# Kernel tuning notes

Hardware: AMD Instinct MI355X
Metric: run time of the kernel (lower is better)

## Reference

```python
import math
import jax, jax.numpy as jnp
import numpy as np

NUM_HEADS = 16
NUM_BUCKETS = 32
MAX_DISTANCE = 128
NEG_INF = -1e9
LN_EPS = 1e-5


def _rel_pos_bias(rab_emb, T):
    # buckets for relative position (i - j) clamped at 0, T5-style log buckets
    i = jnp.arange(T)[:, None]
    j = jnp.arange(T)[None, :]
    n = jnp.clip(i - j, 0, None)  # = -(mem - ctx), clamped min 0
    max_exact = NUM_BUCKETS // 2
    large = max_exact + (
        jnp.log(n.astype(jnp.float32) / max_exact + 1e-6)
        / math.log(MAX_DISTANCE / max_exact)
        * (NUM_BUCKETS - max_exact)
    ).astype(jnp.int32)
    large = jnp.minimum(large, NUM_BUCKETS - 1)
    buckets = jnp.where(n < max_exact, n, large)  # [T, T]
    return rab_emb[buckets].transpose(2, 0, 1)[None]  # [1, H, T, T]


def setup_inputs() -> dict:
    key = jax.random.key(0)
    ks = jax.random.split(key, 8)
    B, T, D = 2, 1024, 1024
    x = jax.random.normal(ks[0], (B, T, D), dtype=jnp.float32)
    # additive causal mask: 0 where allowed, -1e9 where blocked (code tests ==0 for allowed)
    causal_block = jnp.triu(jnp.ones((T, T), dtype=bool), k=1)
    attention_mask = jnp.where(causal_block, NEG_INF, 0.0).astype(jnp.float32)
    # key padding: second sequence has last 256 positions padded
    lengths = jnp.array([T, T - 256])
    key_padding_mask = jnp.arange(T)[None, :] >= lengths[:, None]  # True = pad
    s = 1.0 / math.sqrt(D)
    W_in = jax.random.normal(ks[1], (4 * D, D), dtype=jnp.float32) * s
    b_in = jax.random.normal(ks[2], (4 * D,), dtype=jnp.float32) * 0.02
    W_out = jax.random.normal(ks[3], (D, D), dtype=jnp.float32) * s
    b_out = jax.random.normal(ks[4], (D,), dtype=jnp.float32) * 0.02
    gamma = jnp.ones((D,), dtype=jnp.float32)
    beta = jnp.zeros((D,), dtype=jnp.float32)
    rab_emb = jax.random.normal(ks[5], (NUM_BUCKETS, NUM_HEADS), dtype=jnp.float32) * 0.02
    return {
        "x": x,
        "attention_mask": attention_mask,
        "key_padding_mask": key_padding_mask,
        "W_in": W_in,
        "b_in": b_in,
        "W_out": W_out,
        "b_out": b_out,
        "gamma": gamma,
        "beta": beta,
        "rab_emb": rab_emb,
    }


def reference(x, attention_mask, key_padding_mask, W_in, b_in, W_out, b_out, gamma, beta, rab_emb):
    B, T, D = x.shape
    H = NUM_HEADS
    hd = D // H
    alpha = hd ** (-0.5)

    h = jax.nn.silu(x @ W_in.T + b_in)  # [B, T, 4D]
    U, V, Q, K = jnp.split(h, 4, axis=-1)

    def heads(t):
        return t.reshape(B, T, H, hd).transpose(0, 2, 1, 3)  # [B, H, T, hd]

    Qh, Kh, Vh = heads(Q), heads(K), heads(V)

    rab = _rel_pos_bias(rab_emb, T)  # [1, H, T, T]
    logits = jnp.einsum("bhtd,bhsd->bhts", Qh, Kh) * alpha + rab + attention_mask[None, None]

    valid = (~key_padding_mask).astype(jnp.float32)[:, None, None, :]  # [B,1,1,T]
    allowed = (attention_mask == 0).astype(jnp.float32)[None, None] * valid  # [B,1,T,T] bcast
    # padded keys: torch masked_fill(-inf) then logits_safe -> -1e9
    logits = jnp.where(valid == 0, NEG_INF, logits)

    denom = jnp.clip(jnp.sum(allowed, axis=-1, keepdims=True), 1.0, None)
    attention = jax.nn.silu(logits) / denom  # pointwise SiLU attention, no softmax

    AV = jnp.einsum("bhts,bhsd->bthd", attention, Vh).reshape(B, T, D)

    mu = jnp.mean(AV, axis=-1, keepdims=True)
    var = jnp.var(AV, axis=-1, keepdims=True)
    normed = (AV - mu) / jnp.sqrt(var + LN_EPS) * gamma + beta

    y = (normed * U) @ W_out.T + b_out  # U_flat == U (head reshape round-trips)
    return x + y
```

## Files before the change

### kernel.cpp

```cpp
#include <hip/hip_runtime.h>
#include <stdint.h>

#define DEV static __device__ __forceinline__

typedef unsigned short u16;
typedef float floatx4 __attribute__((ext_vector_type(4)));
typedef short bf16x8 __attribute__((ext_vector_type(8)));

constexpr int Tn = 1024;
constexpr int Dn = 1024;
constexpr int Hn = 16;
constexpr int FD = 4096;

DEV float b2f(u16 u) { union { unsigned int i; float f; } v; v.i = ((unsigned int)u) << 16; return v.f; }
DEV u16 f2b(float f) {
  union { float f; unsigned int i; } v; v.f = f;
  unsigned int x = v.i;
  x += 0x7fffu + ((x >> 16) & 1u);
  return (u16)(x >> 16);
}

DEV void async16(const void* g, void* l) {
  __builtin_amdgcn_global_load_lds((const __attribute__((address_space(1))) void*)g,
                                   (__attribute__((address_space(3))) void*)l,
                                   16, 0, 0);
}

DEV bool is_bf16(const unsigned* gdet) { return gdet[0] == 0x3F803F80u; }
DEV int kp_mode(const unsigned* kp) {
  unsigned d511 = kp[511];
  if (d511 == 0x01010101u) return 1;
  unsigned d1023 = kp[1023];
  if (d1023 == 0x3F803F80u) return 2;
  unsigned d2047 = kp[2047];
  return (d2047 == 0x3F800000u) ? 3 : 0;
}
DEV int nchunks(int qt) { return (qt < 6) ? 1 : ((qt < 12) ? 2 : 3); }

__global__ void prep_all(const void* __restrict__ x, const void* __restrict__ wi,
                         const void* __restrict__ wo, u16* __restrict__ xb,
                         u16* __restrict__ wib, u16* __restrict__ wob,
                         const void* __restrict__ bi, const void* __restrict__ bo,
                         const void* __restrict__ ga, const void* __restrict__ be,
                         const void* __restrict__ kp, const void* __restrict__ rab,
                         float* __restrict__ smallf, float* __restrict__ biasG,
                         float* __restrict__ denomG, unsigned long long* __restrict__ kmaskG)
{
  const unsigned* gdet = (const unsigned*)ga;
  const int bid = blockIdx.x;
  const int tid = threadIdx.x;
  __shared__ unsigned char vb[1024];
  __shared__ int wtot[4];

  if (bid < 1792) {
    if (is_bf16(gdet)) return;
    int i0 = bid * 256 + tid;
#pragma unroll
    for (int k = 0; k < 4; k++) {
      int i = i0 + k * 458752;
      const void* src; u16* dst; int j;
      if (i < 524288)       { src = x;  dst = xb;  j = i; }
      else if (i < 1572864) { src = wi; dst = wib; j = i - 524288; }
      else                  { src = wo; dst = wob; j = i - 1572864; }
      float4 v = ((const float4*)src)[j];
      ushort4 o; o.x = f2b(v.x); o.y = f2b(v.y); o.z = f2b(v.z); o.w = f2b(v.w);
      ((ushort4*)dst)[j] = o;
    }
    return;
  }
  if (bid < 1794) {
    const int b = bid - 1792;
    const int mode = kp_mode((const unsigned*)kp);
    int vv[4];
    const int t0 = tid * 4;
#pragma unroll
    for (int i = 0; i < 4; i++) {
      int t = b * Tn + t0 + i;
      int pad;
      if (mode == 0)      pad = (((const int*)kp)[t] != 0);
      else if (mode == 1) pad = (((const unsigned char*)kp)[t] != 0);
      else if (mode == 2) pad = (((const u16*)kp)[t] != 0);
      else                pad = (((const float*)kp)[t] != 0.f);
      vv[i] = pad ? 0 : 1;
      vb[t0 + i] = (unsigned char)vv[i];
    }
    int p1 = vv[0], p2 = p1 + vv[1], p3 = p2 + vv[2], p4 = p3 + vv[3];
    const int lane = tid & 63, w = tid >> 6;
    int ws = p4;
#pragma unroll
    for (int off = 1; off < 64; off <<= 1) {
      int t = __shfl_up(ws, off, 64);
      if (lane >= off) ws += t;
    }
    if (lane == 63) wtot[w] = ws;
    __syncthreads();
    int base = 0;
    for (int j = 0; j < w; j++) base += wtot[j];
    int excl = base + ws - p4;
    int c1 = excl + p1, c2 = excl + p2, c3 = excl + p3, c4 = excl + p4;
    denomG[b * Tn + t0 + 0] = (float)(c1 < 1 ? 1 : c1);
    denomG[b * Tn + t0 + 1] = (float)(c2 < 1 ? 1 : c2);
    denomG[b * Tn + t0 + 2] = (float)(c3 < 1 ? 1 : c3);
    denomG[b * Tn + t0 + 3] = (float)(c4 < 1 ? 1 : c4);
    if (tid < 16) {
      unsigned long long m = 0;
      for (int j = 0; j < 64; j++) m |= (unsigned long long)vb[tid * 64 + j] << j;
      kmaskG[b * 16 + tid] = m;
    }
    return;
  }
  const bool fbf = is_bf16(gdet);
  for (int i = tid; i < 7168; i += 256) {
    const void* src; int j;
    if (i < 4096)      { src = bi; j = i; }
    else if (i < 5120) { src = bo; j = i - 4096; }
    else if (i < 6144) { src = ga; j = i - 5120; }
    else               { src = be; j = i - 6144; }
    smallf[i] = fbf ? b2f(((const u16*)src)[j]) : ((const float*)src)[j];
  }
  for (int i = tid; i < Hn * Tn; i += 256) {
    int hh = i >> 10, d = i & 1023;
    int bk;
    if (d < 16) bk = d;
    else {
      float lg = logf((float)d * 0.0625f + 1e-6f) / logf(8.f) * 16.f;
      bk = 16 + (int)lg;
      bk = bk < 31 ? bk : 31;
    }
    int j = bk * Hn + hh;
    biasG[i] = fbf ? b2f(((const u16*)rab)[j]) : ((const float*)rab)[j];
  }
}

template<int BM, int BN, int WR, int WC, int EPI>
__global__ __launch_bounds__(WR * WC * 64, 4)
void gemm_bt(const u16* __restrict__ Ac, const u16* __restrict__ Ar,
             const u16* __restrict__ Bc, const u16* __restrict__ Br,
             const float* __restrict__ biasf, void* __restrict__ C,
             u16* __restrict__ VtG, const unsigned* __restrict__ gdet,
             int M, int N, int K)
{
  constexpr int NTH = WR * WC * 64;
  constexpr int MT = BM / (WR * 16);
  constexpr int NTT = BN / (WC * 16);
  __shared__ u16 As[2][BM * 64];
  __shared__ u16 Bs[2][BN * 64];
  const int fbf = is_bf16(gdet) ? 1 : 0;
  const u16* A  = fbf ? Ar : Ac;
  const u16* Bm = fbf ? Br : Bc;
  const int tid = threadIdx.x;
  const int lane = tid & 63;
  const int w = tid >> 6;
  const int wm = w / WC, wn = w % WC;
  const int q = lane >> 4, l16 = lane & 15;
  const int rowBase = blockIdx.y * BM;
  const int colBase = blockIdx.x * BN;
  const int ksl = K / gridDim.z;
  const int kb0 = blockIdx.z * ksl;
  const int nIter = ksl >> 6;

  floatx4 acc[MT][NTT];
#pragma unroll
  for (int i = 0; i < MT; i++)
#pragma unroll
    for (int j = 0; j < NTT; j++)
#pragma unroll
      for (int r = 0; r < 4; r++) acc[i][j][r] = 0.f;

  auto stage = [&](int buf, int kb) {
#pragma unroll
    for (int i = 0; i < BM * 8 / NTH; i++) {
      int c = i * NTH + tid;
      int row = c >> 3, cl = (c & 7) ^ (row & 7);
      async16(&A[(size_t)(rowBase + row) * K + kb + cl * 8], &As[buf][c * 8]);
    }
#pragma unroll
    for (int i = 0; i < BN * 8 / NTH; i++) {
      int c = i * NTH + tid;
      int row = c >> 3, cl = (c & 7) ^ (row & 7);
      async16(&Bm[(size_t)(colBase + row) * K + kb + cl * 8], &Bs[buf][c * 8]);
    }
  };

  stage(0, kb0);
  __syncthreads();

  const int rsw = l16 & 7;
  for (int it = 0; it < nIter; it++) {
    const int cur = it & 1;
    if (it + 1 < nIter) stage(cur ^ 1, kb0 + (it + 1) * 64);
#pragma unroll
    for (int ko = 0; ko < 2; ko++) {
      bf16x8 af[MT], bfr[NTT];
#pragma unroll
      for (int mt = 0; mt < MT; mt++) {
        int row = wm * (MT * 16) + mt * 16 + l16;
        af[mt] = *(const bf16x8*)&As[cur][(row * 8 + ((ko * 4 + q) ^ rsw)) * 8];
      }
#pragma unroll
      for (int nt = 0; nt < NTT; nt++) {
        int row = wn * (NTT * 16) + nt * 16 + l16;
        bfr[nt] = *(const bf16x8*)&Bs[cur][(row * 8 + ((ko * 4 + q) ^ rsw)) * 8];
      }
#pragma unroll
      for (int mt = 0; mt < MT; mt++)
#pragma unroll
        for (int nt = 0; nt < NTT; nt++)
          acc[mt][nt] = __builtin_amdgcn_mfma_f32_16x16x32_bf16(af[mt], bfr[nt], acc[mt][nt], 0, 0, 0);
    }
    __syncthreads();
  }

  const bool isV = (EPI == 0) && (colBase >= Dn) && (colBase < 2 * Dn);
  const size_t pOff = (size_t)blockIdx.z * M * N;
#pragma unroll
  for (int mt = 0; mt < MT; mt++)
#pragma unroll
    for (int nt = 0; nt < NTT; nt++) {
      int col = colBase + wn * (NTT * 16) + nt * 16 + l16;
      float bcol = (EPI == 0) ? biasf[col] : 0.f;
      int row0 = rowBase + wm * (MT * 16) + mt * 16 + q * 4;
      if (EPI == 0) {
        u16 pr[4];
#pragma unroll
        for (int r = 0; r < 4; r++) {
          float v = acc[mt][nt][r] + bcol;
          v = v / (1.f + __expf(-v));
          pr[r] = f2b(v);
        }
        if (isV) {
          int d = col - Dn;
          u16* vp = &VtG[(((size_t)(row0 >> 10) * Hn + (d >> 6)) * 64 + (d & 63)) * Tn + (row0 & 1023)];
          *(uint2*)vp = make_uint2(pr[0] | ((unsigned)pr[1] << 16),
                                   pr[2] | ((unsigned)pr[3] << 16));
        } else {
#pragma unroll
          for (int r = 0; r < 4; r++)
            ((u16*)C)[(size_t)(row0 + r) * N + col] = pr[r];
        }
      } else {
#pragma unroll
        for (int r = 0; r < 4; r++)
          ((float*)C)[pOff + (size_t)(row0 + r) * N + col] = acc[mt][nt][r];
      }
    }
}

__global__ __launch_bounds__(256)
void reduce2(const float* __restrict__ Gp, const void* __restrict__ X,
             const float* __restrict__ bout, void* __restrict__ out,
             const unsigned* __restrict__ gdet)
{
  const int fbf = is_bf16(gdet) ? 1 : 0;
  const int row = blockIdx.x;
  const int tid = threadIdx.x;
  const size_t ridx = (size_t)row * Dn;
  float4 a = ((const float4*)(Gp + ridx))[tid];
  float4 p = ((const float4*)(Gp + 2097152 + ridx))[tid];
  a.x += p.x; a.y += p.y; a.z += p.z; a.w += p.w;
  float4 bb = ((const float4*)bout)[tid];
  a.x += bb.x; a.y += bb.y; a.z += bb.z; a.w += bb.w;
  if (fbf) {
    ushort4 xv = ((const ushort4*)X)[ridx / 4 + tid];
    a.x += b2f(xv.x); a.y += b2f(xv.y); a.z += b2f(xv.z); a.w += b2f(xv.w);
    ushort4 o; o.x = f2b(a.x); o.y = f2b(a.y); o.z = f2b(a.z); o.w = f2b(a.w);
    ((ushort4*)out)[ridx / 4 + tid] = o;
  } else {
    float4 xv = ((const float4*)X)[ridx / 4 + tid];
    a.x += xv.x; a.y += xv.y; a.z += xv.z; a.w += xv.w;
    ((float4*)out)[ridx / 4 + tid] = a;
  }
}

__global__ __launch_bounds__(256, 4)
void attn_kern(const u16* __restrict__ h, const u16* __restrict__ VtG,
               const float* __restrict__ biasG, const float* __restrict__ denomG,
               const unsigned long long* __restrict__ kmaskG,
               float* __restrict__ AV)
{
  __shared__ u16 Qs[4096];
  __shared__ u16 Ks[4096];
  __shared__ u16 Vs[4096];
  __shared__ u16 Ps[4096];
  __shared__ float biasL[1024];
  const int tid = threadIdx.x;
  const int lane = tid & 63;
  const int w = tid >> 6;
  const int q = lane >> 4, l16 = lane & 15;

  int qt = 0, rem = blockIdx.x;
  for (;;) { int P = nchunks(qt); if (rem < P) break; rem -= P; qt++; }
  const int c = rem;
  const int P = nchunks(qt);
  const int n = qt + 1, cb = n / P, cr = n % P;
  const int kt0 = c * cb + (c < cr ? c : cr);
  const int kt1 = kt0 + cb + (c < cr ? 1 : 0);

  const int head = blockIdx.y, b = blockIdx.z;
  const u16* hb = h + (size_t)b * Tn * FD;
  const u16* vtb = VtG + ((size_t)(b * Hn + head)) * 64 * Tn;

#pragma unroll
  for (int i = 0; i < 2; i++) {
    int s = i * 256 + tid;
    int row = s >> 3, dc = (s & 7) ^ (row & 7);
    async16(&hb[(size_t)(qt * 64 + row) * FD + 2048 + head * 64 + dc * 8], &Qs[s * 8]);
    async16(&hb[(size_t)(kt0 * 64 + row) * FD + 3072 + head * 64 + dc * 8], &Ks[s * 8]);
    async16(&vtb[(size_t)row * Tn + kt0 * 64 + dc * 8], &Vs[s * 8]);
  }
  async16(&biasG[head * Tn + tid * 4], &biasL[tid * 4]);
  __syncthreads();

  const int sw0 = q ^ (l16 & 7);
  const int qrow = w * 16 + l16;
  bf16x8 bq0 = *(const bf16x8*)&Qs[(qrow * 8 + sw0) * 8];
  bf16x8 bq1 = *(const bf16x8*)&Qs[(qrow * 8 + (sw0 ^ 4)) * 8];
  const float dinv = 1.f / denomG[b * Tn + qt * 64 + qrow];

  floatx4 o[4];
#pragma unroll
  for (int nt = 0; nt < 4; nt++)
#pragma unroll
    for (int r = 0; r < 4; r++) o[nt][r] = 0.f;

  for (int kt = kt0; kt < kt1; kt++) {
    const unsigned long long km = kmaskG[b * 16 + kt];
    const int dq = (qt - kt) * 64 + qrow;
#pragma unroll
    for (int st = 0; st < 4; st++) {
      int rk = (st * 16 + l16) * 8;
      bf16x8 ak0 = *(const bf16x8*)&Ks[(rk + sw0) * 8];
      bf16x8 ak1 = *(const bf16x8*)&Ks[(rk + (sw0 ^ 4)) * 8];
      floatx4 sT;
#pragma unroll
      for (int r = 0; r < 4; r++) sT[r] = 0.f;
      sT = __builtin_amdgcn_mfma_f32_16x16x32_bf16(ak0, bq0, sT, 0, 0, 0);
      sT = __builtin_amdgcn_mfma_f32_16x16x32_bf16(ak1, bq1, sT, 0, 0, 0);
      unsigned mb = (unsigned)(km >> (st * 16 + q * 4)) & 0xFu;
      u16 pr[4];
#pragma unroll
      for (int r = 0; r < 4; r++) {
        int delta = dq - (st * 16 + q * 4 + r);
        float p = 0.f;
        if (((mb >> r) & 1u) && delta >= 0) {
          float xv = sT[r] * 0.125f + biasL[delta];
          p = xv * dinv / (1.f + __expf(-xv));
        }
        pr[r] = f2b(p);
      }
      unsigned lo = pr[0] | ((unsigned)pr[1] << 16);
      unsigned hi = pr[2] | ((unsigned)pr[3] << 16);
      int cch = (st * 2 + (q >> 1)) ^ (l16 & 7);
      *(uint2*)&Ps[w * 1024 + l16 * 64 + cch * 8 + (q & 1) * 4] = make_uint2(lo, hi);
    }
    int rp = w * 1024 + l16 * 64;
    bf16x8 ap0 = *(const bf16x8*)&Ps[rp + sw0 * 8];
    bf16x8 ap1 = *(const bf16x8*)&Ps[rp + (sw0 ^ 4) * 8];
#pragma unroll
    for (int nt = 0; nt < 4; nt++) {
      int rv = (nt * 16 + l16) * 8;
      bf16x8 bv0 = *(const bf16x8*)&Vs[(rv + sw0) * 8];
      bf16x8 bv1 = *(const bf16x8*)&Vs[(rv + (sw0 ^ 4)) * 8];
      o[nt] = __builtin_amdgcn_mfma_f32_16x16x32_bf16(ap0, bv0, o[nt], 0, 0, 0);
      o[nt] = __builtin_amdgcn_mfma_f32_16x16x32_bf16(ap1, bv1, o[nt], 0, 0, 0);
    }
    if (kt + 1 < kt1) {
      __syncthreads();
#pragma unroll
      for (int i = 0; i < 2; i++) {
        int s = i * 256 + tid;
        int row = s >> 3, dc = (s & 7) ^ (row & 7);
        async16(&hb[(size_t)((kt + 1) * 64 + row) * FD + 3072 + head * 64 + dc * 8], &Ks[s * 8]);
        async16(&vtb[(size_t)row * Tn + (kt + 1) * 64 + dc * 8], &Vs[s * 8]);
      }
      __syncthreads();
    }
  }

  float* avp = AV + (size_t)c * 2097152
             + ((size_t)b * Tn + qt * 64 + w * 16 + q * 4) * Dn + head * 64;
#pragma unroll
  for (int nt = 0; nt < 4; nt++)
#pragma unroll
    for (int r = 0; r < 4; r++)
      avp[(size_t)r * Dn + nt * 16 + l16] = o[nt][r];
}

__global__ __launch_bounds__(256)
void ln_mul(const float* __restrict__ AV, const u16* __restrict__ h,
            const float* __restrict__ gam, const float* __restrict__ bet,
            u16* __restrict__ z)
{
  struct alignas(8) U4 { u16 a, b, c, d; };
  const int row = blockIdx.x;
  const int tid = threadIdx.x;
  const int P = nchunks(row >> 6 & 15);
  float4 v = ((const float4*)(AV + (size_t)row * Dn))[tid];
  if (P > 1) {
    float4 p = ((const float4*)(AV + 2097152 + (size_t)row * Dn))[tid];
    v.x += p.x; v.y += p.y; v.z += p.z; v.w += p.w;
  }
  if (P > 2) {
    float4 p = ((const float4*)(AV + 4194304 + (size_t)row * Dn))[tid];
    v.x += p.x; v.y += p.y; v.z += p.z; v.w += p.w;
  }
  float s  = v.x + v.y + v.z + v.w;
  float s2 = v.x * v.x + v.y * v.y + v.z * v.z + v.w * v.w;
#pragma unroll
  for (int off = 32; off > 0; off >>= 1) {
    s  += __shfl_down(s, off, 64);
    s2 += __shfl_down(s2, off, 64);
  }
  __shared__ float red[8];
  const int lane = tid & 63, w = tid >> 6;
  if (lane == 0) { red[w] = s; red[4 + w] = s2; }
  __syncthreads();
  const float su = red[0] + red[1] + red[2] + red[3];
  const float sq = red[4] + red[5] + red[6] + red[7];
  const float mu = su * (1.f / 1024.f);
  const float var = sq * (1.f / 1024.f) - mu * mu;
  const float rstd = rsqrtf(var + 1e-5f);

  const U4 uu = ((const U4*)(h + (size_t)row * FD))[tid];
  const float4 g4 = ((const float4*)gam)[tid];
  const float4 b4 = ((const float4*)bet)[tid];
  float r0 = ((v.x - mu) * rstd * g4.x + b4.x) * b2f(uu.a);
  float r1 = ((v.y - mu) * rstd * g4.y + b4.y) * b2f(uu.b);
  float r2 = ((v.z - mu) * rstd * g4.z + b4.z) * b2f(uu.c);
  float r3 = ((v.w - mu) * rstd * g4.w + b4.w) * b2f(uu.d);
  U4 outv; outv.a = f2b(r0); outv.b = f2b(r1); outv.c = f2b(r2); outv.d = f2b(r3);
  ((U4*)(z + (size_t)row * Dn))[tid] = outv;
}

extern "C" void kernel_launch(void* const* d_in, const int* in_sizes, int n_in,
                              void* d_out, int out_size, void* d_ws, size_t ws_size,
                              hipStream_t stream)
{
  const void* x     = d_in[0];
  const void* kp    = d_in[2];
  const void* W_in  = d_in[3];
  const void* b_in  = d_in[4];
  const void* W_out = d_in[5];
  const void* b_out = d_in[6];
  const void* gamma = d_in[7];
  const void* beta  = d_in[8];
  const void* rab   = d_in[9];
  const unsigned* gdet = (const unsigned*)gamma;

  char* ws = (char*)d_ws;
  u16*   h     = (u16*)(ws);
  float* AV    = (float*)(ws + 16777216);
  float* Gp    = (float*)(ws);
  u16*   z     = (u16*)(ws + 41943040);
  u16*   xb    = (u16*)(ws + 46137344);
  u16*   Wib   = (u16*)(ws + 50331648);
  u16*   Wob   = (u16*)(ws + 58720256);
  u16*   VtG   = (u16*)(ws + 60817408);
  float* smallf= (float*)(ws + 65011712);
  float* biasG = (float*)(ws + 65040384);
  float* denom = (float*)(ws + 65105920);
  unsigned long long* kmask = (unsigned long long*)(ws + 65114112);

  prep_all<<<1795, 256, 0, stream>>>(x, W_in, W_out, xb, Wib, Wob,
                                     b_in, b_out, gamma, beta, kp, rab,
                                     smallf, biasG, denom, kmask);
  gemm_bt<128, 128, 4, 2, 0><<<dim3(32, 16, 1), dim3(512), 0, stream>>>(
      xb, (const u16*)x, Wib, (const u16*)W_in, smallf, h, VtG, gdet, 2048, 4096, 1024);
  attn_kern<<<dim3(30, 16, 2), dim3(256), 0, stream>>>(h, VtG, biasG, denom, kmask, AV);
  ln_mul<<<2048, 256, 0, stream>>>(AV, h, smallf + 5120, smallf + 6144, z);
  gemm_bt<128, 64, 4, 2, 2><<<dim3(16, 16, 2), dim3(512), 0, stream>>>(
      z, z, Wob, (const u16*)W_out, smallf, Gp, nullptr, gdet, 2048, 1024, 1024);
  reduce2<<<2048, 256, 0, stream>>>(Gp, x, smallf + 4096, d_out, gdet);
}
```

Baseline: 181.3 us.

## Fuse output GEMM epilogue, double-buffer attention K/V, reduce attention split chunks

The output projection GEMM now runs without split-K at a 64x64 tile and adds the bias and the residual x directly in its epilogue, so the separate reduce2 kernel and the partial-sum buffer are gone. The attention kernel double-buffers K/V tiles in LDS, prefetching the next tile before computing the current one, and reuses the Q buffer for P to make room. The key range is now split into at most 2 chunks instead of 3, giving 24 blocks per head in the grid. Occupancy is lowered to 3 blocks per SM because LDS use grows, and the GEMM without split-K does longer K loops per block.

```diff
diff --git a/kernel.cpp b/kernel.cpp
--- a/kernel.cpp
+++ b/kernel.cpp
@@ -35,7 +35,7 @@
   unsigned d2047 = kp[2047];
   return (d2047 == 0x3F800000u) ? 3 : 0;
 }
-DEV int nchunks(int qt) { return (qt < 6) ? 1 : ((qt < 12) ? 2 : 3); }
+DEV int nchunks(int qt) { return (qt < 8) ? 1 : 2; }
 
 __global__ void prep_all(const void* __restrict__ x, const void* __restrict__ wi,
                          const void* __restrict__ wo, u16* __restrict__ xb,
@@ -136,9 +136,9 @@
 __global__ __launch_bounds__(WR * WC * 64, 4)
 void gemm_bt(const u16* __restrict__ Ac, const u16* __restrict__ Ar,
              const u16* __restrict__ Bc, const u16* __restrict__ Br,
-             const float* __restrict__ biasf, void* __restrict__ C,
-             u16* __restrict__ VtG, const unsigned* __restrict__ gdet,
-             int M, int N, int K)
+             const float* __restrict__ biasf, const void* __restrict__ X,
+             void* __restrict__ C, u16* __restrict__ VtG,
+             const unsigned* __restrict__ gdet, int M, int N, int K)
 {
   constexpr int NTH = WR * WC * 64;
   constexpr int MT = BM / (WR * 16);
@@ -155,9 +155,7 @@
   const int q = lane >> 4, l16 = lane & 15;
   const int rowBase = blockIdx.y * BM;
   const int colBase = blockIdx.x * BN;
-  const int ksl = K / gridDim.z;
-  const int kb0 = blockIdx.z * ksl;
-  const int nIter = ksl >> 6;
+  const int nIter = K >> 6;
 
   floatx4 acc[MT][NTT];
 #pragma unroll
@@ -182,13 +180,13 @@
     }
   };
 
-  stage(0, kb0);
+  stage(0, 0);
   __syncthreads();
 
   const int rsw = l16 & 7;
   for (int it = 0; it < nIter; it++) {
     const int cur = it & 1;
-    if (it + 1 < nIter) stage(cur ^ 1, kb0 + (it + 1) * 64);
+    if (it + 1 < nIter) stage(cur ^ 1, (it + 1) * 64);
 #pragma unroll
     for (int ko = 0; ko < 2; ko++) {
       bf16x8 af[MT], bfr[NTT];
@@ -212,13 +210,12 @@
   }
 
   const bool isV = (EPI == 0) && (colBase >= Dn) && (colBase < 2 * Dn);
-  const size_t pOff = (size_t)blockIdx.z * M * N;
 #pragma unroll
   for (int mt = 0; mt < MT; mt++)
 #pragma unroll
     for (int nt = 0; nt < NTT; nt++) {
       int col = colBase + wn * (NTT * 16) + nt * 16 + l16;
-      float bcol = (EPI == 0) ? biasf[col] : 0.f;
+      float bcol = biasf[col];
       int row0 = rowBase + wm * (MT * 16) + mt * 16 + q * 4;
       if (EPI == 0) {
         u16 pr[4];
@@ -240,48 +237,30 @@
         }
       } else {
 #pragma unroll
-        for (int r = 0; r < 4; r++)
-          ((float*)C)[pOff + (size_t)(row0 + r) * N + col] = acc[mt][nt][r];
+        for (int r = 0; r < 4; r++) {
+          size_t idx = (size_t)(row0 + r) * N + col;
+          float v = acc[mt][nt][r] + bcol;
+          if (fbf) {
+            v += b2f(((const u16*)X)[idx]);
+            ((u16*)C)[idx] = f2b(v);
+          } else {
+            v += ((const float*)X)[idx];
+            ((float*)C)[idx] = v;
+          }
+        }
       }
     }
 }
 
-__global__ __launch_bounds__(256)
-void reduce2(const float* __restrict__ Gp, const void* __restrict__ X,
-             const float* __restrict__ bout, void* __restrict__ out,
-             const unsigned* __restrict__ gdet)
-{
-  const int fbf = is_bf16(gdet) ? 1 : 0;
-  const int row = blockIdx.x;
-  const int tid = threadIdx.x;
-  const size_t ridx = (size_t)row * Dn;
-  float4 a = ((const float4*)(Gp + ridx))[tid];
-  float4 p = ((const float4*)(Gp + 2097152 + ridx))[tid];
-  a.x += p.x; a.y += p.y; a.z += p.z; a.w += p.w;
-  float4 bb = ((const float4*)bout)[tid];
-  a.x += bb.x; a.y += bb.y; a.z += bb.z; a.w += bb.w;
-  if (fbf) {
-    ushort4 xv = ((const ushort4*)X)[ridx / 4 + tid];
-    a.x += b2f(xv.x); a.y += b2f(xv.y); a.z += b2f(xv.z); a.w += b2f(xv.w);
-    ushort4 o; o.x = f2b(a.x); o.y = f2b(a.y); o.z = f2b(a.z); o.w = f2b(a.w);
-    ((ushort4*)out)[ridx / 4 + tid] = o;
-  } else {
-    float4 xv = ((const float4*)X)[ridx / 4 + tid];
-    a.x += xv.x; a.y += xv.y; a.z += xv.z; a.w += xv.w;
-    ((float4*)out)[ridx / 4 + tid] = a;
-  }
-}
-
-__global__ __launch_bounds__(256, 4)
+__global__ __launch_bounds__(256, 3)
 void attn_kern(const u16* __restrict__ h, const u16* __restrict__ VtG,
                const float* __restrict__ biasG, const float* __restrict__ denomG,
                const unsigned long long* __restrict__ kmaskG,
                float* __restrict__ AV)
 {
-  __shared__ u16 Qs[4096];
-  __shared__ u16 Ks[4096];
-  __shared__ u16 Vs[4096];
-  __shared__ u16 Ps[4096];
+  __shared__ u16 QPs[4096];
+  __shared__ u16 Ks[2][4096];
+  __shared__ u16 Vs[2][4096];
   __shared__ float biasL[1024];
   const int tid = threadIdx.x;
   const int lane = tid & 63;
@@ -304,17 +283,17 @@
   for (int i = 0; i < 2; i++) {
     int s = i * 256 + tid;
     int row = s >> 3, dc = (s & 7) ^ (row & 7);
-    async16(&hb[(size_t)(qt * 64 + row) * FD + 2048 + head * 64 + dc * 8], &Qs[s * 8]);
-    async16(&hb[(size_t)(kt0 * 64 + row) * FD + 3072 + head * 64 + dc * 8], &Ks[s * 8]);
-    async16(&vtb[(size_t)row * Tn + kt0 * 64 + dc * 8], &Vs[s * 8]);
+    async16(&hb[(size_t)(qt * 64 + row) * FD + 2048 + head * 64 + dc * 8], &QPs[s * 8]);
+    async16(&hb[(size_t)(kt0 * 64 + row) * FD + 3072 + head * 64 + dc * 8], &Ks[0][s * 8]);
+    async16(&vtb[(size_t)row * Tn + kt0 * 64 + dc * 8], &Vs[0][s * 8]);
   }
   async16(&biasG[head * Tn + tid * 4], &biasL[tid * 4]);
   __syncthreads();
 
   const int sw0 = q ^ (l16 & 7);
   const int qrow = w * 16 + l16;
-  bf16x8 bq0 = *(const bf16x8*)&Qs[(qrow * 8 + sw0) * 8];
-  bf16x8 bq1 = *(const bf16x8*)&Qs[(qrow * 8 + (sw0 ^ 4)) * 8];
+  bf16x8 bq0 = *(const bf16x8*)&QPs[(qrow * 8 + sw0) * 8];
+  bf16x8 bq1 = *(const bf16x8*)&QPs[(qrow * 8 + (sw0 ^ 4)) * 8];
   const float dinv = 1.f / denomG[b * Tn + qt * 64 + qrow];
 
   floatx4 o[4];
@@ -323,14 +302,26 @@
 #pragma unroll
     for (int r = 0; r < 4; r++) o[nt][r] = 0.f;
 
+  int buf = 0;
   for (int kt = kt0; kt < kt1; kt++) {
+    if (kt + 1 < kt1) {
+      int nb = buf ^ 1;
+      int krow = (kt + 1) * 64;
+#pragma unroll
+      for (int i = 0; i < 2; i++) {
+        int s = i * 256 + tid;
+        int row = s >> 3, dc = (s & 7) ^ (row & 7);
+        async16(&hb[(size_t)(krow + row) * FD + 3072 + head * 64 + dc * 8], &Ks[nb][s * 8]);
+        async16(&vtb[(size_t)row * Tn + krow + dc * 8], &Vs[nb][s * 8]);
+      }
+    }
     const unsigned long long km = kmaskG[b * 16 + kt];
     const int dq = (qt - kt) * 64 + qrow;
 #pragma unroll
     for (int st = 0; st < 4; st++) {
       int rk = (st * 16 + l16) * 8;
-      bf16x8 ak0 = *(const bf16x8*)&Ks[(rk + sw0) * 8];
-      bf16x8 ak1 = *(const bf16x8*)&Ks[(rk + (sw0 ^ 4)) * 8];
+      bf16x8 ak0 = *(const bf16x8*)&Ks[buf][(rk + sw0) * 8];
+      bf16x8 ak1 = *(const bf16x8*)&Ks[buf][(rk + (sw0 ^ 4)) * 8];
       floatx4 sT;
 #pragma unroll
       for (int r = 0; r < 4; r++) sT[r] = 0.f;
@@ -351,30 +342,21 @@
       unsigned lo = pr[0] | ((unsigned)pr[1] << 16);
       unsigned hi = pr[2] | ((unsigned)pr[3] << 16);
       int cch = (st * 2 + (q >> 1)) ^ (l16 & 7);
-      *(uint2*)&Ps[w * 1024 + l16 * 64 + cch * 8 + (q & 1) * 4] = make_uint2(lo, hi);
+      *(uint2*)&QPs[w * 1024 + l16 * 64 + cch * 8 + (q & 1) * 4] = make_uint2(lo, hi);
     }
     int rp = w * 1024 + l16 * 64;
-    bf16x8 ap0 = *(const bf16x8*)&Ps[rp + sw0 * 8];
-    bf16x8 ap1 = *(const bf16x8*)&Ps[rp + (sw0 ^ 4) * 8];
+    bf16x8 ap0 = *(const bf16x8*)&QPs[rp + sw0 * 8];
+    bf16x8 ap1 = *(const bf16x8*)&QPs[rp + (sw0 ^ 4) * 8];
 #pragma unroll
     for (int nt = 0; nt < 4; nt++) {
       int rv = (nt * 16 + l16) * 8;
-      bf16x8 bv0 = *(const bf16x8*)&Vs[(rv + sw0) * 8];
-      bf16x8 bv1 = *(const bf16x8*)&Vs[(rv + (sw0 ^ 4)) * 8];
+      bf16x8 bv0 = *(const bf16x8*)&Vs[buf][(rv + sw0) * 8];
+      bf16x8 bv1 = *(const bf16x8*)&Vs[buf][(rv + (sw0 ^ 4)) * 8];
       o[nt] = __builtin_amdgcn_mfma_f32_16x16x32_bf16(ap0, bv0, o[nt], 0, 0, 0);
       o[nt] = __builtin_amdgcn_mfma_f32_16x16x32_bf16(ap1, bv1, o[nt], 0, 0, 0);
     }
-    if (kt + 1 < kt1) {
-      __syncthreads();
-#pragma unroll
-      for (int i = 0; i < 2; i++) {
-        int s = i * 256 + tid;
-        int row = s >> 3, dc = (s & 7) ^ (row & 7);
-        async16(&hb[(size_t)((kt + 1) * 64 + row) * FD + 3072 + head * 64 + dc * 8], &Ks[s * 8]);
-        async16(&vtb[(size_t)row * Tn + (kt + 1) * 64 + dc * 8], &Vs[s * 8]);
-      }
-      __syncthreads();
-    }
+    if (kt + 1 < kt1) __syncthreads();
+    buf ^= 1;
   }
 
   float* avp = AV + (size_t)c * 2097152
@@ -398,10 +380,6 @@
   float4 v = ((const float4*)(AV + (size_t)row * Dn))[tid];
   if (P > 1) {
     float4 p = ((const float4*)(AV + 2097152 + (size_t)row * Dn))[tid];
-    v.x += p.x; v.y += p.y; v.z += p.z; v.w += p.w;
-  }
-  if (P > 2) {
-    float4 p = ((const float4*)(AV + 4194304 + (size_t)row * Dn))[tid];
     v.x += p.x; v.y += p.y; v.z += p.z; v.w += p.w;
   }
   float s  = v.x + v.y + v.z + v.w;
@@ -450,7 +428,6 @@
   char* ws = (char*)d_ws;
   u16*   h     = (u16*)(ws);
   float* AV    = (float*)(ws + 16777216);
-  float* Gp    = (float*)(ws);
   u16*   z     = (u16*)(ws + 41943040);
   u16*   xb    = (u16*)(ws + 46137344);
   u16*   Wib   = (u16*)(ws + 50331648);
@@ -465,10 +442,11 @@
                                      b_in, b_out, gamma, beta, kp, rab,
                                      smallf, biasG, denom, kmask);
   gemm_bt<128, 128, 4, 2, 0><<<dim3(32, 16, 1), dim3(512), 0, stream>>>(
-      xb, (const u16*)x, Wib, (const u16*)W_in, smallf, h, VtG, gdet, 2048, 4096, 1024);
-  attn_kern<<<dim3(30, 16, 2), dim3(256), 0, stream>>>(h, VtG, biasG, denom, kmask, AV);
+      xb, (const u16*)x, Wib, (const u16*)W_in, smallf, nullptr,
+      h, VtG, gdet, 2048, 4096, 1024);
+  attn_kern<<<dim3(24, 16, 2), dim3(256), 0, stream>>>(h, VtG, biasG, denom, kmask, AV);
   ln_mul<<<2048, 256, 0, stream>>>(AV, h, smallf + 5120, smallf + 6144, z);
-  gemm_bt<128, 64, 4, 2, 2><<<dim3(16, 16, 2), dim3(512), 0, stream>>>(
-      z, z, Wob, (const u16*)W_out, smallf, Gp, nullptr, gdet, 2048, 1024, 1024);
-  reduce2<<<2048, 256, 0, stream>>>(Gp, x, smallf + 4096, d_out, gdet);
-}
+  gemm_bt<64, 64, 4, 2, 1><<<dim3(16, 32, 1), dim3(512), 0, stream>>>(
+      z, z, Wob, (const u16*)W_out, smallf + 4096, x, d_out, nullptr,
+      gdet, 2048, 1024, 1024);
+}
```

Result: no change. 183.1 us (+1.0%).
